# Performance work log

Measured on AMD Instinct MI355X. Metric: run time of the kernel, lower is better.

## Reference

```python
import jax, jax.numpy as jnp
import numpy as np

B, S, E, H = 4, 1024, 1024, 16
D = E // H  # head dim = 64

def setup_inputs() -> dict:
    key = jax.random.key(0)
    k1, k2, k3, k4, k5 = jax.random.split(key, 5)
    return {
        "lstm_out": jax.random.normal(k1, (B, S, E), dtype=jnp.float32),
        "in_proj_weight": jax.random.normal(k2, (3 * E, E), dtype=jnp.float32) * 0.02,
        "in_proj_bias": jax.random.normal(k3, (3 * E,), dtype=jnp.float32) * 0.02,
        "out_proj_weight": jax.random.normal(k4, (E, E), dtype=jnp.float32) * 0.02,
        "out_proj_bias": jax.random.normal(k5, (E,), dtype=jnp.float32) * 0.02,
    }

def reference(lstm_out, in_proj_weight, in_proj_bias, out_proj_weight, out_proj_bias):
    # Packed QKV projection, as in nn.MultiheadAttention (Linear uses x @ W.T + b)
    qkv = lstm_out @ in_proj_weight.T + in_proj_bias          # [B,S,3E]
    q, k, v = jnp.split(qkv, 3, axis=-1)                      # each [B,S,E]
    def heads(t):
        return t.reshape(B, S, H, D).transpose(0, 2, 1, 3)    # [B,H,S,D]
    q, k, v = heads(q), heads(k), heads(v)
    scale = 1.0 / jnp.sqrt(jnp.asarray(D, dtype=q.dtype))
    scores = jnp.einsum("bhsd,bhtd->bhst", q * scale, k)      # [B,H,S,S]
    attn = jax.nn.softmax(scores, axis=-1)                    # [B,H,S,S]
    ctx = jnp.einsum("bhst,bhtd->bhsd", attn, v)              # [B,H,S,D]
    ctx = ctx.transpose(0, 2, 1, 3).reshape(B, S, E)          # [B,S,E]
    attn_output = ctx @ out_proj_weight.T + out_proj_bias     # [B,S,E]
    # need_weights=True with default average_attn_weights=True -> mean over heads
    attn_weights = attn.mean(axis=1)                          # [B,S,S]
    context_vector = attn_output.mean(axis=1)                 # [B,E]
    return (context_vector, attn_weights)
```

## Files before the change

### kernel.cpp

```cpp
#include <hip/hip_runtime.h>


typedef unsigned short u16;
using s16x8 = __attribute__((ext_vector_type(8))) short;
using f32x4 = __attribute__((ext_vector_type(4))) float;
using u16x4 = __attribute__((ext_vector_type(4))) unsigned short;

#define AS1 __attribute__((address_space(1)))
#define AS3 __attribute__((address_space(3)))

#define QSCALE 0.1803368801111204f

__device__ __forceinline__ u16 f2bf(float f) {
    unsigned u = __float_as_uint(f);
    u += 0x7fffu + ((u >> 16) & 1u);
    return (u16)(u >> 16);
}

__global__ void k_prep(const float* __restrict__ X, const float* __restrict__ W1,
                       u16* __restrict__ Xb, u16* __restrict__ W1b,
                       float* __restrict__ cmean) {
    int i = blockIdx.x * blockDim.x + threadIdx.x;
    const float* src; u16* dst; int off;
    if (i < 1048576)       { src = X;  dst = Xb;  off = i; }
    else                   { src = W1; dst = W1b; off = i - 1048576; }
    float4 v = reinterpret_cast<const float4*>(src)[off];
    u16x4 o = { f2bf(v.x), f2bf(v.y), f2bf(v.z), f2bf(v.w) };
    reinterpret_cast<u16x4*>(dst)[off] = o;
    if (i < 4096) cmean[i] = 0.f;
}

__global__ __launch_bounds__(512) void k_gemm_bt(
    const u16* __restrict__ A, const u16* __restrict__ B,
    const float* __restrict__ bias, u16* __restrict__ C,
    u16* __restrict__ vt) {
    const int K = 1024;
    const int nbx = gridDim.x;
    const int nwg = nbx * gridDim.y;
    const int bid = blockIdx.y * nbx + blockIdx.x;
    const int per = nwg >> 3;
    const int swz = (bid & 7) * per + (bid >> 3);
    const int n0 = (swz % nbx) * 128, m0 = (swz / nbx) * 128;
    const int tid = threadIdx.x, lane = tid & 63, w = tid >> 6;
    const int wm = w >> 1, wn = w & 1;
    const int g = lane >> 4, l15 = lane & 15;
    __shared__ __attribute__((aligned(16))) u16 As[2][128 * 64];
    __shared__ __attribute__((aligned(16))) u16 Bs[2][128 * 64];

    f32x4 acc[2][4];
    #pragma unroll
    for (int mi = 0; mi < 2; ++mi)
        #pragma unroll
        for (int nj = 0; nj < 4; ++nj) acc[mi][nj] = (f32x4){0.f, 0.f, 0.f, 0.f};

    auto STAGE = [&](int k0, int sb) {
        #pragma unroll
        for (int r = 0; r < 2; ++r) {
            int c = tid + r * 512;
            int row = c >> 3, j = c & 7;
            int js = j ^ (row & 7);
            __builtin_amdgcn_global_load_lds(
                (AS1 const void*)(A + (size_t)(m0 + row) * K + k0 + js * 8),
                (AS3 void*)(&As[sb][c * 8]), 16, 0, 0);
            __builtin_amdgcn_global_load_lds(
                (AS1 const void*)(B + (size_t)(n0 + row) * K + k0 + js * 8),
                (AS3 void*)(&Bs[sb][c * 8]), 16, 0, 0);
        }
    };

    STAGE(0, 0);
    int buf = 0;
    for (int k0 = 0; k0 < K; k0 += 64) {
        __syncthreads();
        if (k0 + 64 < K) STAGE(k0 + 64, buf ^ 1);
        #pragma unroll
        for (int kk = 0; kk < 64; kk += 32) {
            const int cx0 = (((kk >> 3) + g) ^ (l15 & 7)) * 8;
            s16x8 av[2], bv[4];
            #pragma unroll
            for (int mi = 0; mi < 2; ++mi)
                av[mi] = *reinterpret_cast<const s16x8*>(
                    &As[buf][(wm * 32 + mi * 16 + l15) * 64 + cx0]);
            #pragma unroll
            for (int nj = 0; nj < 4; ++nj)
                bv[nj] = *reinterpret_cast<const s16x8*>(
                    &Bs[buf][(wn * 64 + nj * 16 + l15) * 64 + cx0]);
            #pragma unroll
            for (int mi = 0; mi < 2; ++mi)
                #pragma unroll
                for (int nj = 0; nj < 4; ++nj)
                    acc[mi][nj] = __builtin_amdgcn_mfma_f32_16x16x32_bf16(av[mi], bv[nj], acc[mi][nj], 0, 0, 0);
        }
        buf ^= 1;
    }

    #pragma unroll
    for (int nj = 0; nj < 4; ++nj) {
        int n = n0 + wn * 64 + nj * 16 + l15;
        float scale = (n < 1024) ? QSCALE : 1.0f;
        float bvs = bias[n] * scale;
        if (n < 2048) {
            #pragma unroll
            for (int mi = 0; mi < 2; ++mi)
                #pragma unroll
                for (int i = 0; i < 4; ++i) {
                    int m = m0 + wm * 32 + mi * 16 + g * 4 + i;
                    C[(size_t)m * 2048 + n] = f2bf(acc[mi][nj][i] * scale + bvs);
                }
        } else {
            int hd = n - 2048;
            #pragma unroll
            for (int mi = 0; mi < 2; ++mi)
                #pragma unroll
                for (int i = 0; i < 4; ++i) {
                    int m = m0 + wm * 32 + mi * 16 + g * 4 + i;
                    int b = m >> 10, t = m & 1023;
                    vt[((size_t)(b * 16 + (hd >> 6)) * 64 + (hd & 63)) * 1024 + t] =
                        f2bf(acc[mi][nj][i] + bvs);
                }
        }
    }
}

__global__ __launch_bounds__(256, 4) void k_flash(const u16* __restrict__ qk,
                                                  const u16* __restrict__ vt,
                                                  float* __restrict__ ml,
                                                  float* __restrict__ cmean) {
    const int id = blockIdx.x + 16 * (blockIdx.y + 16 * blockIdx.z);
    const int x = id & 7, kq = id >> 3;
    const int gbh = x * 8 + (kq >> 4);
    const int qt = kq & 15;
    const int b = gbh >> 4, h = gbh & 15;
    const int q0 = qt * 64;
    const int tid = threadIdx.x, lane = tid & 63, w = tid >> 6;
    const int g = lane >> 4, l15 = lane & 15;
    __shared__ __attribute__((aligned(16))) u16 Ks[2][64 * 64];
    __shared__ __attribute__((aligned(16))) u16 Vt[2][64 * 64];
    __shared__ __attribute__((aligned(16))) u16 Ps[4][16 * 64];

    const size_t rowQ = (size_t)(b * 1024 + q0 + w * 16 + l15) * 2048 + h * 64;
    const s16x8 qa0 = *reinterpret_cast<const s16x8*>(qk + rowQ + g * 8);
    const s16x8 qa1 = *reinterpret_cast<const s16x8*>(qk + rowQ + 32 + g * 8);
    const s16x8 onesv = { (short)0x3F80, (short)0x3F80, (short)0x3F80, (short)0x3F80,
                          (short)0x3F80, (short)0x3F80, (short)0x3F80, (short)0x3F80 };

    const int cA = tid, cB = tid + 256;
    const int rowA = cA >> 3, jA = cA & 7, rowB = cB >> 3, jB = cB & 7;
    const u16* kbase0 = qk + (size_t)(b * 1024) * 2048 + 1024 + h * 64;
    const u16* vtb = vt + (size_t)(b * 16 + h) * 65536;

    __builtin_amdgcn_global_load_lds((AS1 const void*)(kbase0 + (size_t)rowA * 2048 + ((jA ^ (rowA & 7)) * 8)),
                                     (AS3 void*)(&Ks[0][cA * 8]), 16, 0, 0);
    __builtin_amdgcn_global_load_lds((AS1 const void*)(kbase0 + (size_t)rowB * 2048 + ((jB ^ (rowB & 7)) * 8)),
                                     (AS3 void*)(&Ks[0][cB * 8]), 16, 0, 0);
    __builtin_amdgcn_global_load_lds((AS1 const void*)(vtb + (size_t)rowA * 1024 + ((jA ^ (rowA & 7)) * 8)),
                                     (AS3 void*)(&Vt[0][cA * 8]), 16, 0, 0);
    __builtin_amdgcn_global_load_lds((AS1 const void*)(vtb + (size_t)rowB * 1024 + ((jB ^ (rowB & 7)) * 8)),
                                     (AS3 void*)(&Vt[0][cB * 8]), 16, 0, 0);

    f32x4 ctxa[4];
    #pragma unroll
    for (int nj = 0; nj < 4; ++nj) ctxa[nj] = (f32x4){0.f, 0.f, 0.f, 0.f};
    f32x4 lacc = (f32x4){0.f, 0.f, 0.f, 0.f};

    int buf = 0;
    for (int kt = 0; kt < 16; ++kt) {
        __syncthreads();
        if (kt < 15) {
            int t0n = (kt + 1) * 64;
            const u16* kbase = kbase0 + (size_t)t0n * 2048;
            __builtin_amdgcn_global_load_lds((AS1 const void*)(kbase + (size_t)rowA * 2048 + ((jA ^ (rowA & 7)) * 8)),
                                             (AS3 void*)(&Ks[buf ^ 1][cA * 8]), 16, 0, 0);
            __builtin_amdgcn_global_load_lds((AS1 const void*)(kbase + (size_t)rowB * 2048 + ((jB ^ (rowB & 7)) * 8)),
                                             (AS3 void*)(&Ks[buf ^ 1][cB * 8]), 16, 0, 0);
            const u16* vbase = vtb + t0n;
            __builtin_amdgcn_global_load_lds((AS1 const void*)(vbase + (size_t)rowA * 1024 + ((jA ^ (rowA & 7)) * 8)),
                                             (AS3 void*)(&Vt[buf ^ 1][cA * 8]), 16, 0, 0);
            __builtin_amdgcn_global_load_lds((AS1 const void*)(vbase + (size_t)rowB * 1024 + ((jB ^ (rowB & 7)) * 8)),
                                             (AS3 void*)(&Vt[buf ^ 1][cB * 8]), 16, 0, 0);
        }

        f32x4 sc[4];
        #pragma unroll
        for (int tj = 0; tj < 4; ++tj) sc[tj] = (f32x4){0.f, 0.f, 0.f, 0.f};
        __builtin_amdgcn_s_setprio(1);
        #pragma unroll
        for (int kk = 0; kk < 64; kk += 32) {
            s16x8 qa = kk ? qa1 : qa0;
            #pragma unroll
            for (int tj = 0; tj < 4; ++tj) {
                int trow = tj * 16 + l15;
                s16x8 kb = *reinterpret_cast<const s16x8*>(
                    &Ks[buf][trow * 64 + ((((kk >> 3) + g) ^ (trow & 7)) * 8)]);
                sc[tj] = __builtin_amdgcn_mfma_f32_16x16x32_bf16(kb, qa, sc[tj], 0, 0, 0);
            }
        }
        __builtin_amdgcn_s_setprio(0);

        #pragma unroll
        for (int tj = 0; tj < 4; ++tj)
            #pragma unroll
            for (int i = 0; i < 4; ++i)
                sc[tj][i] = exp2f(sc[tj][i]);

        #pragma unroll
        for (int tj = 0; tj < 4; ++tj) {
            unsigned pk01, pk23;
            asm("v_cvt_pk_bf16_f32 %0, %1, %2" : "=v"(pk01) : "v"(sc[tj][0]), "v"(sc[tj][1]));
            asm("v_cvt_pk_bf16_f32 %0, %1, %2" : "=v"(pk23) : "v"(sc[tj][2]), "v"(sc[tj][3]));
            uint2 pk = { pk01, pk23 };
            *reinterpret_cast<uint2*>(
                &Ps[w][l15 * 64 + (((tj * 2 + (g >> 1)) ^ (l15 & 7)) * 8) + (g & 1) * 4]) = pk;
        }

        __builtin_amdgcn_s_setprio(1);
        #pragma unroll
        for (int kk = 0; kk < 64; kk += 32) {
            s16x8 pa = *reinterpret_cast<const s16x8*>(
                &Ps[w][l15 * 64 + ((((kk >> 3) + g) ^ (l15 & 7)) * 8)]);
            lacc = __builtin_amdgcn_mfma_f32_16x16x32_bf16(pa, onesv, lacc, 0, 0, 0);
            #pragma unroll
            for (int nj = 0; nj < 4; ++nj) {
                int d = nj * 16 + l15;
                s16x8 vb = *reinterpret_cast<const s16x8*>(
                    &Vt[buf][d * 64 + ((((kk >> 3) + g) ^ (d & 7)) * 8)]);
                ctxa[nj] = __builtin_amdgcn_mfma_f32_16x16x32_bf16(pa, vb, ctxa[nj], 0, 0, 0);
            }
        }
        __builtin_amdgcn_s_setprio(0);
        buf ^= 1;
    }

    float inv_i[4];
    #pragma unroll
    for (int i = 0; i < 4; ++i) {
        inv_i[i] = 1.0f / lacc[i];
        if (l15 == 0)
            ml[(size_t)(b * 16 + h) * 1024 + q0 + w * 16 + g * 4 + i] = inv_i[i] * 0.0625f;
    }

    #pragma unroll
    for (int nj = 0; nj < 4; ++nj) {
        float s = ctxa[nj][0] * inv_i[0] + ctxa[nj][1] * inv_i[1]
                + ctxa[nj][2] * inv_i[2] + ctxa[nj][3] * inv_i[3];
        s += __shfl_xor(s, 16);
        s += __shfl_xor(s, 32);
        if (g == 0)
            atomicAdd(&cmean[b * 1024 + h * 64 + nj * 16 + l15], s * (1.0f / 1024.0f));
    }
}

__global__ __launch_bounds__(256, 4) void k_attnw(const u16* __restrict__ qk,
                                                  const float* __restrict__ ml,
                                                  float* __restrict__ attnw) {
    const int tt = blockIdx.x, stp = blockIdx.y, b = blockIdx.z;
    const int s0a = stp * 128, t0 = tt * 64;
    const int tid = threadIdx.x, lane = tid & 63, w = tid >> 6;
    const int g = lane >> 4, l15 = lane & 15;
    __shared__ __attribute__((aligned(16))) u16 Ks[2][64 * 64];
    __shared__ float mls[16][128];

    #pragma unroll
    for (int r = 0; r < 8; ++r) {
        int idx = tid + r * 256;
        int hh = idx >> 7, row = idx & 127;
        mls[hh][row] = ml[(size_t)(b * 16 + hh) * 1024 + s0a + row];
    }

    const int cA = tid, cB = tid + 256;
    const int rowA = cA >> 3, jA = cA & 7, rowB = cB >> 3, jB = cB & 7;
    const u16* kbase = qk + (size_t)(b * 1024 + t0) * 2048 + 1024;
    const size_t rowQa = (size_t)(b * 1024 + s0a + w * 16 + l15) * 2048;
    const size_t rowQb = rowQa + (size_t)64 * 2048;

    __builtin_amdgcn_global_load_lds((AS1 const void*)(kbase + (size_t)rowA * 2048 + ((jA ^ (rowA & 7)) * 8)),
                                     (AS3 void*)(&Ks[0][cA * 8]), 16, 0, 0);
    __builtin_amdgcn_global_load_lds((AS1 const void*)(kbase + (size_t)rowB * 2048 + ((jB ^ (rowB & 7)) * 8)),
                                     (AS3 void*)(&Ks[0][cB * 8]), 16, 0, 0);
    s16x8 qcA0 = *reinterpret_cast<const s16x8*>(qk + rowQa + g * 8);
    s16x8 qcA1 = *reinterpret_cast<const s16x8*>(qk + rowQa + 32 + g * 8);
    s16x8 qcB0 = *reinterpret_cast<const s16x8*>(qk + rowQb + g * 8);
    s16x8 qcB1 = *reinterpret_cast<const s16x8*>(qk + rowQb + 32 + g * 8);

    f32x4 accA[4], accB[4];
    #pragma unroll
    for (int tj = 0; tj < 4; ++tj) {
        accA[tj] = (f32x4){0.f, 0.f, 0.f, 0.f};
        accB[tj] = (f32x4){0.f, 0.f, 0.f, 0.f};
    }

    int buf = 0;
    for (int h = 0; h < 16; ++h) {
        __syncthreads();
        s16x8 qnA0, qnA1, qnB0, qnB1;
        if (h < 15) {
            const u16* kb2 = kbase + (h + 1) * 64;
            __builtin_amdgcn_global_load_lds((AS1 const void*)(kb2 + (size_t)rowA * 2048 + ((jA ^ (rowA & 7)) * 8)),
                                             (AS3 void*)(&Ks[buf ^ 1][cA * 8]), 16, 0, 0);
            __builtin_amdgcn_global_load_lds((AS1 const void*)(kb2 + (size_t)rowB * 2048 + ((jB ^ (rowB & 7)) * 8)),
                                             (AS3 void*)(&Ks[buf ^ 1][cB * 8]), 16, 0, 0);
            qnA0 = *reinterpret_cast<const s16x8*>(qk + rowQa + (h + 1) * 64 + g * 8);
            qnA1 = *reinterpret_cast<const s16x8*>(qk + rowQa + (h + 1) * 64 + 32 + g * 8);
            qnB0 = *reinterpret_cast<const s16x8*>(qk + rowQb + (h + 1) * 64 + g * 8);
            qnB1 = *reinterpret_cast<const s16x8*>(qk + rowQb + (h + 1) * 64 + 32 + g * 8);
        }

        f32x4 scA[4], scB[4];
        #pragma unroll
        for (int tj = 0; tj < 4; ++tj) {
            scA[tj] = (f32x4){0.f, 0.f, 0.f, 0.f};
            scB[tj] = (f32x4){0.f, 0.f, 0.f, 0.f};
        }
        #pragma unroll
        for (int kk = 0; kk < 64; kk += 32) {
            s16x8 qaA = kk ? qcA1 : qcA0;
            s16x8 qaB = kk ? qcB1 : qcB0;
            #pragma unroll
            for (int tj = 0; tj < 4; ++tj) {
                int trow = tj * 16 + l15;
                s16x8 kb = *reinterpret_cast<const s16x8*>(
                    &Ks[buf][trow * 64 + ((((kk >> 3) + g) ^ (trow & 7)) * 8)]);
                scA[tj] = __builtin_amdgcn_mfma_f32_16x16x32_bf16(qaA, kb, scA[tj], 0, 0, 0);
                scB[tj] = __builtin_amdgcn_mfma_f32_16x16x32_bf16(qaB, kb, scB[tj], 0, 0, 0);
            }
        }
        #pragma unroll
        for (int i = 0; i < 4; ++i) {
            int row = w * 16 + g * 4 + i;
            float Ma = mls[h][row];
            float Mb = mls[h][64 + row];
            #pragma unroll
            for (int tj = 0; tj < 4; ++tj) {
                accA[tj][i] += exp2f(scA[tj][i]) * Ma;
                accB[tj][i] += exp2f(scB[tj][i]) * Mb;
            }
        }
        qcA0 = qnA0; qcA1 = qnA1; qcB0 = qnB0; qcB1 = qnB1;
        buf ^= 1;
    }

    #pragma unroll
    for (int i = 0; i < 4; ++i) {
        int rowa = s0a + w * 16 + g * 4 + i;
        #pragma unroll
        for (int tj = 0; tj < 4; ++tj) {
            attnw[(size_t)(b * 1024 + rowa) * 1024 + t0 + tj * 16 + l15] = accA[tj][i];
            attnw[(size_t)(b * 1024 + rowa + 64) * 1024 + t0 + tj * 16 + l15] = accB[tj][i];
        }
    }
}

__global__ __launch_bounds__(256) void k_outproj(const float* __restrict__ cmean,
                                                 const float* __restrict__ wout,
                                                 const float* __restrict__ bias,
                                                 float* __restrict__ out) {
    __shared__ float cs[4096];
    #pragma unroll
    for (int r = 0; r < 16; ++r) {
        int idx = threadIdx.x + r * 256;
        cs[idx] = cmean[idx];
    }
    __syncthreads();
    int G = blockIdx.x * 256 + threadIdx.x;
    int e = G >> 4, ks = G & 15;
    const float4* wr = reinterpret_cast<const float4*>(wout) + (size_t)e * 256 + ks * 16;
    const float4* c0 = reinterpret_cast<const float4*>(&cs[0]) + ks * 16;
    const float4* c1 = reinterpret_cast<const float4*>(&cs[1024]) + ks * 16;
    const float4* c2 = reinterpret_cast<const float4*>(&cs[2048]) + ks * 16;
    const float4* c3 = reinterpret_cast<const float4*>(&cs[3072]) + ks * 16;
    float s0 = 0.f, s1 = 0.f, s2 = 0.f, s3 = 0.f;
    #pragma unroll
    for (int k = 0; k < 16; ++k) {
        float4 wv = wr[k];
        float4 a = c0[k], b = c1[k], c = c2[k], d = c3[k];
        s0 += a.x * wv.x + a.y * wv.y + a.z * wv.z + a.w * wv.w;
        s1 += b.x * wv.x + b.y * wv.y + b.z * wv.z + b.w * wv.w;
        s2 += c.x * wv.x + c.y * wv.y + c.z * wv.z + c.w * wv.w;
        s3 += d.x * wv.x + d.y * wv.y + d.z * wv.z + d.w * wv.w;
    }
    #pragma unroll
    for (int off = 1; off < 16; off <<= 1) {
        s0 += __shfl_xor(s0, off);
        s1 += __shfl_xor(s1, off);
        s2 += __shfl_xor(s2, off);
        s3 += __shfl_xor(s3, off);
    }
    if (ks == 0) {
        float bv = bias[e];
        out[e]        = s0 + bv;
        out[1024 + e] = s1 + bv;
        out[2048 + e] = s2 + bv;
        out[3072 + e] = s3 + bv;
    }
}

extern "C" void kernel_launch(void* const* d_in, const int* in_sizes, int n_in,
                              void* d_out, int out_size, void* d_ws, size_t ws_size,
                              hipStream_t stream) {
    const float* lstm = (const float*)d_in[0];
    const float* wqkv = (const float*)d_in[1];
    const float* bqkv = (const float*)d_in[2];
    const float* wout = (const float*)d_in[3];
    const float* bout = (const float*)d_in[4];
    float* out = (float*)d_out;

    char* ws = (char*)d_ws;
    u16*   Xbf   = (u16*)(ws);
    u16*   Wqkvb = (u16*)(ws + 8u  * 1024 * 1024);
    u16*   qkbuf = (u16*)(ws + 16u * 1024 * 1024);
    u16*   vtg   = (u16*)(ws + 32u * 1024 * 1024);
    float* ml    = (float*)(ws + 40u * 1024 * 1024);
    float* cmean = (float*)(ws + 41u * 1024 * 1024);

    k_prep<<<7168, 256, 0, stream>>>(lstm, wqkv, Xbf, Wqkvb, cmean);

    k_gemm_bt<<<dim3(24, 32), 512, 0, stream>>>(Xbf, Wqkvb, bqkv, qkbuf, vtg);
    k_flash<<<dim3(16, 16, 4), 256, 0, stream>>>(qkbuf, vtg, ml, cmean);
    k_attnw<<<dim3(16, 8, 4), 256, 0, stream>>>(qkbuf, ml, out + 4096);
    k_outproj<<<64, 256, 0, stream>>>(cmean, wout, bout, out);
}
```

Before: 121.5 us.

## Switch QKV GEMM to 32x32x16 MFMA with 4 waves per block

Rewrites the QKV projection GEMM to use 32x32x16 bf16 MFMA tiles, with each of 4 waves computing a 64x64 sub-tile, instead of 8 waves each computing 32x64 with 16x16x32 MFMA. Block size drops from 512 to 256 threads, and each thread now stages four LDS chunks per K-step. The aim is fewer LDS fragment reads per MFMA and better register reuse from larger per-wave tiles. The trade-off is fewer waves available to hide latency and more accumulator registers per thread. The epilogue row mapping is updated for the 32x32 output layout.

```diff
diff --git a/kernel.cpp b/kernel.cpp
--- a/kernel.cpp
+++ b/kernel.cpp
@@ -2,9 +2,10 @@
 
 
 typedef unsigned short u16;
-using s16x8 = __attribute__((ext_vector_type(8))) short;
-using f32x4 = __attribute__((ext_vector_type(4))) float;
-using u16x4 = __attribute__((ext_vector_type(4))) unsigned short;
+using s16x8  = __attribute__((ext_vector_type(8)))  short;
+using f32x4  = __attribute__((ext_vector_type(4)))  float;
+using f32x16 = __attribute__((ext_vector_type(16))) float;
+using u16x4  = __attribute__((ext_vector_type(4)))  unsigned short;
 
 #define AS1 __attribute__((address_space(1)))
 #define AS3 __attribute__((address_space(3)))
@@ -30,7 +31,7 @@
     if (i < 4096) cmean[i] = 0.f;
 }
 
-__global__ __launch_bounds__(512) void k_gemm_bt(
+__global__ __launch_bounds__(256) void k_gemm_bt(
     const u16* __restrict__ A, const u16* __restrict__ B,
     const float* __restrict__ bias, u16* __restrict__ C,
     u16* __restrict__ vt) {
@@ -43,20 +44,22 @@
     const int n0 = (swz % nbx) * 128, m0 = (swz / nbx) * 128;
     const int tid = threadIdx.x, lane = tid & 63, w = tid >> 6;
     const int wm = w >> 1, wn = w & 1;
-    const int g = lane >> 4, l15 = lane & 15;
+    const int l31 = lane & 31, g2 = lane >> 5;
     __shared__ __attribute__((aligned(16))) u16 As[2][128 * 64];
     __shared__ __attribute__((aligned(16))) u16 Bs[2][128 * 64];
 
-    f32x4 acc[2][4];
+    f32x16 acc[2][2];
     #pragma unroll
     for (int mi = 0; mi < 2; ++mi)
         #pragma unroll
-        for (int nj = 0; nj < 4; ++nj) acc[mi][nj] = (f32x4){0.f, 0.f, 0.f, 0.f};
+        for (int ni = 0; ni < 2; ++ni)
+            #pragma unroll
+            for (int r = 0; r < 16; ++r) acc[mi][ni][r] = 0.f;
 
     auto STAGE = [&](int k0, int sb) {
         #pragma unroll
-        for (int r = 0; r < 2; ++r) {
-            int c = tid + r * 512;
+        for (int r = 0; r < 4; ++r) {
+            int c = tid + r * 256;
             int row = c >> 3, j = c & 7;
             int js = j ^ (row & 7);
             __builtin_amdgcn_global_load_lds(
@@ -74,49 +77,52 @@
         __syncthreads();
         if (k0 + 64 < K) STAGE(k0 + 64, buf ^ 1);
         #pragma unroll
-        for (int kk = 0; kk < 64; kk += 32) {
-            const int cx0 = (((kk >> 3) + g) ^ (l15 & 7)) * 8;
-            s16x8 av[2], bv[4];
+        for (int ks = 0; ks < 4; ++ks) {
+            const int cx = ((ks * 2 + g2) ^ (l31 & 7)) * 8;
+            s16x8 av[2], bv[2];
             #pragma unroll
             for (int mi = 0; mi < 2; ++mi)
                 av[mi] = *reinterpret_cast<const s16x8*>(
-                    &As[buf][(wm * 32 + mi * 16 + l15) * 64 + cx0]);
-            #pragma unroll
-            for (int nj = 0; nj < 4; ++nj)
-                bv[nj] = *reinterpret_cast<const s16x8*>(
-                    &Bs[buf][(wn * 64 + nj * 16 + l15) * 64 + cx0]);
+                    &As[buf][(wm * 64 + mi * 32 + l31) * 64 + cx]);
+            #pragma unroll
+            for (int ni = 0; ni < 2; ++ni)
+                bv[ni] = *reinterpret_cast<const s16x8*>(
+                    &Bs[buf][(wn * 64 + ni * 32 + l31) * 64 + cx]);
             #pragma unroll
             for (int mi = 0; mi < 2; ++mi)
                 #pragma unroll
-                for (int nj = 0; nj < 4; ++nj)
-                    acc[mi][nj] = __builtin_amdgcn_mfma_f32_16x16x32_bf16(av[mi], bv[nj], acc[mi][nj], 0, 0, 0);
+                for (int ni = 0; ni < 2; ++ni)
+                    acc[mi][ni] = __builtin_amdgcn_mfma_f32_32x32x16_bf16(
+                        av[mi], bv[ni], acc[mi][ni], 0, 0, 0);
         }
         buf ^= 1;
     }
 
     #pragma unroll
-    for (int nj = 0; nj < 4; ++nj) {
-        int n = n0 + wn * 64 + nj * 16 + l15;
+    for (int ni = 0; ni < 2; ++ni) {
+        int n = n0 + wn * 64 + ni * 32 + l31;
         float scale = (n < 1024) ? QSCALE : 1.0f;
         float bvs = bias[n] * scale;
         if (n < 2048) {
             #pragma unroll
             for (int mi = 0; mi < 2; ++mi)
                 #pragma unroll
-                for (int i = 0; i < 4; ++i) {
-                    int m = m0 + wm * 32 + mi * 16 + g * 4 + i;
-                    C[(size_t)m * 2048 + n] = f2bf(acc[mi][nj][i] * scale + bvs);
+                for (int r = 0; r < 16; ++r) {
+                    int rowl = (r & 3) + 8 * (r >> 2) + 4 * g2;
+                    int m = m0 + wm * 64 + mi * 32 + rowl;
+                    C[(size_t)m * 2048 + n] = f2bf(acc[mi][ni][r] * scale + bvs);
                 }
         } else {
             int hd = n - 2048;
             #pragma unroll
             for (int mi = 0; mi < 2; ++mi)
                 #pragma unroll
-                for (int i = 0; i < 4; ++i) {
-                    int m = m0 + wm * 32 + mi * 16 + g * 4 + i;
+                for (int r = 0; r < 16; ++r) {
+                    int rowl = (r & 3) + 8 * (r >> 2) + 4 * g2;
+                    int m = m0 + wm * 64 + mi * 32 + rowl;
                     int b = m >> 10, t = m & 1023;
                     vt[((size_t)(b * 16 + (hd >> 6)) * 64 + (hd & 63)) * 1024 + t] =
-                        f2bf(acc[mi][nj][i] + bvs);
+                        f2bf(acc[mi][ni][r] + bvs);
                 }
         }
     }
@@ -414,7 +420,7 @@
 
     k_prep<<<7168, 256, 0, stream>>>(lstm, wqkv, Xbf, Wqkvb, cmean);
 
-    k_gemm_bt<<<dim3(24, 32), 512, 0, stream>>>(Xbf, Wqkvb, bqkv, qkbuf, vtg);
+    k_gemm_bt<<<dim3(24, 32), 256, 0, stream>>>(Xbf, Wqkvb, bqkv, qkbuf, vtg);
     k_flash<<<dim3(16, 16, 4), 256, 0, stream>>>(qkbuf, vtg, ml, cmean);
     k_attnw<<<dim3(16, 8, 4), 256, 0, stream>>>(qkbuf, ml, out + 4096);
     k_outproj<<<64, 256, 0, stream>>>(cmean, wout, bout, out);
```

After: 127.5 us. +4.9%, slower.
